# Kernel tuning notes

Hardware: AMD Instinct MI355X
Metric: run time of the kernel (lower is better)

## Reference

```python
import jax, jax.numpy as jnp
import numpy as np
from jax.scipy.linalg import solve_triangular

B = 131072; OBS = 128; AD = 8; H = 64; FH = 32; NL = 4
D1 = AD // 2; D2 = AD - D1; TRIL = AD * (AD + 1) // 2
_rows, _cols = np.tril_indices(AD)          # same row-major order as torch.tril_indices
_diag = (_rows == _cols)                    # bool mask over TRIL entries
_diag_pos = np.where(_diag)[0]
LOG2PI = float(np.log(2.0 * np.pi))
EPS = float(np.finfo(np.float32).eps)       # torch RMSNorm default eps = finfo.eps


def _rms(x, w):
    return x * jax.lax.rsqrt(jnp.mean(x * x, axis=-1, keepdims=True) + EPS) * w


def setup_inputs() -> dict:
    ks = iter(jax.random.split(jax.random.key(0), 32))
    def w(shape, scale):
        return jax.random.normal(next(ks), shape, jnp.float32) * scale
    z = lambda *s: jnp.zeros(s, jnp.float32)
    return dict(
        x=jax.random.normal(next(ks), (B, OBS), jnp.float32),
        action=jax.random.normal(next(ks), (B, AD), jnp.float32),
        z_rpo=jax.random.uniform(next(ks), (B, AD), jnp.float32, -0.1, 0.1),
        cW1=w((OBS, H), OBS ** -0.5), cb1=z(H), c_rms=jnp.ones(H, jnp.float32),
        cW2=w((H, H), H ** -0.5), cb2=z(H), cW3=w((H, 1), H ** -0.5), cb3=z(1),
        aW1=w((OBS, H), OBS ** -0.5), ab1=z(H), aW2=w((H, H), H ** -0.5), ab2=z(H),
        mW=w((H, AD), 0.01), mb=z(AD),
        tW1=w((OBS, H), OBS ** -0.5), tb1=z(H), t_rms1=jnp.ones(H, jnp.float32),
        tW2=w((H, H), H ** -0.5), tb2=z(H), t_rms2=jnp.ones(H, jnp.float32),
        hW=w((H, TRIL), 0.01), hb=z(TRIL),
        fW1=w((NL, D1 + OBS, FH), (D1 + OBS) ** -0.5), fb1=z(NL, FH),
        fW2=w((NL, FH, 2 * D2), 0.01), fb2=z(NL, 2 * D2),
    )


def reference(x, action, z_rpo, cW1, cb1, c_rms, cW2, cb2, cW3, cb3,
              aW1, ab1, aW2, ab2, mW, mb,
              tW1, tb1, t_rms1, tW2, tb2, t_rms2, hW, hb,
              fW1, fb1, fW2, fb2):
    silu = jax.nn.silu
    Bn = x.shape[0]
    # actor mean trunk + head, with RPO uniform perturbation (action is given)
    h = silu(silu(x @ aW1 + ab1) @ aW2 + ab2)
    action_mean = h @ mW + mb + z_rpo
    # state-dependent lower-triangular covariance factor
    tl = _rms(silu(x @ tW1 + tb1), t_rms1)
    tl = _rms(silu(tl @ tW2 + tb2), t_rms2)
    raw = tl @ hW + hb                                   # [B, TRIL]
    proc = jnp.where(_diag, jax.nn.softplus(raw), raw)
    L = jnp.zeros((Bn, AD, AD), raw.dtype).at[:, _rows, _cols].set(proc)
    log_det_L = jnp.log(proc[:, _diag_pos]).sum(-1)      # [B]
    # coupling flow inverse: noise -> correlated
    noise = action - action_mean
    x1, x2 = noise[:, :D1], noise[:, D1:]
    fld = jnp.zeros((Bn,), raw.dtype)
    for i in reversed(range(NL)):
        cond, y = (x1, x2) if i % 2 == 0 else (x2, x1)
        st = silu(jnp.concatenate([cond, x], -1) @ fW1[i] + fb1[i]) @ fW2[i] + fb2[i]
        s_raw, tshift = jnp.split(st, 2, -1)
        s = jnp.tanh(s_raw) * 2.0
        xt = (y - tshift) * jnp.exp(-s)
        if i % 2 == 0:
            x2 = xt
        else:
            x1 = xt
        fld = fld + s.sum(-1)
    correlated = jnp.concatenate([x1, x2], -1)           # [B, AD]
    zc = solve_triangular(L, correlated[..., None], lower=True)[..., 0]
    mahal = (zc * zc).sum(-1)
    log_prob = -0.5 * (AD * LOG2PI + mahal) - log_det_L - fld
    entropy = 0.5 * (AD * (1.0 + LOG2PI)) + log_det_L + fld
    # critic
    v = _rms(silu(x @ cW1 + cb1), c_rms)
    v = silu(v @ cW2 + cb2) @ cW3 + cb3                  # [B, 1]
    return (action, log_prob, entropy, v)
```

## Files before the change

kernel.cpp:

```cpp
#include <hip/hip_runtime.h>

typedef __attribute__((ext_vector_type(8))) short    v8s;
typedef __attribute__((ext_vector_type(4))) float    f4;
typedef __attribute__((ext_vector_type(2))) float    f2;
typedef __attribute__((ext_vector_type(2))) unsigned u32x2;

#define MFMA16 __builtin_amdgcn_mfma_f32_16x16x32_bf16

#define AW1T 0
#define TW1T 8192
#define CW1T 16384
#define AW2T 24576
#define TW2T 28672
#define CW2T 32768
#define MWT  36864
#define HWT  37888
#define FW1XT 40960
#define FW2T  57344
#define WS_BF16_TOTAL 59392
#define W1CTO 0
#define HBPO  512

#define LOG2PI 1.83787706640934548356f
#define EPSF   1.1920928955078125e-07f

__device__ __constant__ int PERM[36] = {0,2,5,9,14,20,27,35,
  1,3,4,6,7,8,10,11,12,13,15,16,17,18,19,21,22,23,24,25,26,28,29,30,31,32,33,34};

__device__ __forceinline__ float ubits(unsigned u){union{unsigned u;float f;}c;c.u=u;return c.f;}
__device__ __forceinline__ unsigned fbits(float f){union{float f;unsigned u;}c;c.f=f;return c.u;}
__device__ __forceinline__ float rcpf(float x){ return __builtin_amdgcn_rcpf(x); }
__device__ __forceinline__ float siluf(float v){ return v * rcpf(1.f + __expf(-v)); }
__device__ __forceinline__ unsigned pk2(float a,float b){
  unsigned ua=fbits(a); ua+=0x7fffu+((ua>>16)&1u);
  unsigned ub=fbits(b); ub+=0x7fffu+((ub>>16)&1u);
  return (ua>>16)|(ub&0xffff0000u);
}
__device__ __forceinline__ unsigned short f2bu(float a){
  unsigned ua=fbits(a); ua+=0x7fffu+((ua>>16)&1u);
  return (unsigned short)(ua>>16);
}
__device__ __forceinline__ float b2f16(unsigned short h){ return ubits(((unsigned)h)<<16); }
__device__ __forceinline__ float qsum(float v){
  v += __shfl_xor(v,16,64); v += __shfl_xor(v,32,64); return v;
}
__device__ __forceinline__ int swz(int row, int blk){ return row*64 + ((blk ^ (row&7))*8); }
__device__ __forceinline__ int swzx(int row, int blk){ return row*128 + ((blk ^ (row&7))*8); }

__global__ __launch_bounds__(256)
void prep_kernel(const float* __restrict__ aW1, const float* __restrict__ aW2,
                 const float* __restrict__ mW,  const float* __restrict__ tW1,
                 const float* __restrict__ tW2, const float* __restrict__ hW,
                 const float* __restrict__ hb,  const float* __restrict__ cW1,
                 const float* __restrict__ cW2, const float* __restrict__ fW1,
                 const float* __restrict__ fW2,
                 unsigned short* __restrict__ ws16, float* __restrict__ wsf)
{
  const int tid = blockIdx.x*256 + threadIdx.x;
  const int stride = gridDim.x*256;
  for (int idx=tid; idx<64*128; idx+=stride){
    int f=idx>>9, r=idx&511, lane=r>>3, j=idx&7;
    int wt=f>>2, kt=f&3, c=lane&15, q=lane>>4;
    int n=wt*16+c, k=kt*32+q*8+j;
    ws16[AW1T+idx]=f2bu(aW1[k*64+n]);
    ws16[TW1T+idx]=f2bu(tW1[k*64+n]);
    ws16[CW1T+idx]=f2bu(cW1[k*64+n]);
  }
  for (int idx=tid; idx<64*64; idx+=stride){
    int f=idx>>9, r=idx&511, lane=r>>3, j=idx&7;
    int wt=f>>1, kt=f&1, c=lane&15, q=lane>>4;
    int n=wt*16+c, k=kt*32+q*8+j;
    ws16[AW2T+idx]=f2bu(aW2[k*64+n]);
    ws16[TW2T+idx]=f2bu(tW2[k*64+n]);
    ws16[CW2T+idx]=f2bu(cW2[k*64+n]);
  }
  for (int idx=tid; idx<16*64; idx+=stride){
    int f=idx>>9, r=idx&511, lane=r>>3, j=idx&7;
    int kt=f, c=lane&15, q=lane>>4;
    int n=c, k=kt*32+q*8+j;
    ws16[MWT+idx]=f2bu(n<8 ? mW[k*8+n] : 0.f);
  }
  for (int idx=tid; idx<48*64; idx+=stride){
    int f=idx>>9, r=idx&511, lane=r>>3, j=idx&7;
    int wt=f>>1, kt=f&1, c=lane&15, q=lane>>4;
    int n=wt*16+c, k=kt*32+q*8+j;
    ws16[HWT+idx]=f2bu(n<36 ? hW[k*36+PERM[n]] : 0.f);
  }
  for (int idx=tid; idx<4*32*128; idx+=stride){
    int i=idx>>12, rem=idx&4095;
    int f=rem>>9, r=rem&511, lane=r>>3, j=idx&7;
    int wt=f>>2, kt=f&3, c=lane&15, q=lane>>4;
    int n=wt*16+c, k=kt*32+q*8+j;
    ws16[FW1XT+idx]=f2bu(fW1[i*4224 + (4+k)*32 + n]);
  }
  for (int idx=tid; idx<4*16*32; idx+=stride){
    int i=idx>>9, r=idx&511, lane=r>>3, j=idx&7;
    int c=lane&15, q=lane>>4;
    int k=q*8+j;
    ws16[FW2T+idx]=f2bu(c<8 ? fW2[i*256 + k*8 + c] : 0.f);
  }
  for (int idx=tid; idx<4*32*4; idx+=stride){
    int i=idx>>7, rem=idx&127, n=rem>>2, k=rem&3;
    wsf[W1CTO+idx]=fW1[i*4224 + k*32 + n];
  }
  for (int idx=tid; idx<48; idx+=stride)
    wsf[HBPO+idx] = idx<36 ? hb[PERM[idx]] : 0.f;
}

template<int NWT>
__device__ __forceinline__ void gemmX(const unsigned short* __restrict__ Wt,
                                      const v8s* __restrict__ xf,
                                      f4 (*acc)[2], int lane)
{
#pragma unroll
  for (int kt=0; kt<4; ++kt){
    v8s wf[NWT];
#pragma unroll
    for (int wt=0; wt<NWT; ++wt)
      wf[wt] = *(const v8s*)(Wt + ((wt*4 + kt)*64 + lane)*8);
#pragma unroll
    for (int wt=0; wt<NWT; ++wt)
#pragma unroll
      for (int et=0; et<2; ++et)
        acc[wt][et] = MFMA16(wf[wt], xf[et*4+kt], acc[wt][et], 0,0,0);
  }
}

template<int NWT>
__device__ __forceinline__ void gemmH(const unsigned short* __restrict__ Wt,
                                      const unsigned short* __restrict__ actL,
                                      f4 (*acc)[2], int lane, int c, int q)
{
#pragma unroll
  for (int kt=0; kt<2; ++kt){
    v8s wf[NWT];
#pragma unroll
    for (int wt=0; wt<NWT; ++wt)
      wf[wt] = *(const v8s*)(Wt + ((wt*2 + kt)*64 + lane)*8);
    v8s af[2];
#pragma unroll
    for (int et=0; et<2; ++et)
      af[et] = *(const v8s*)(actL + swz(et*16+c, kt*4+q));
#pragma unroll
    for (int wt=0; wt<NWT; ++wt)
#pragma unroll
      for (int et=0; et<2; ++et)
        acc[wt][et] = MFMA16(wf[wt], af[et], acc[wt][et], 0,0,0);
  }
}

__global__ __launch_bounds__(64) __attribute__((amdgpu_waves_per_eu(3, 4)))
void policy_kernel(
    const float* __restrict__ x,    const float* __restrict__ action, const float* __restrict__ z_rpo,
    const float* __restrict__ cb1,  const float* __restrict__ c_rms,  const float* __restrict__ cb2,
    const float* __restrict__ cW3,  const float* __restrict__ cb3,
    const float* __restrict__ ab1,  const float* __restrict__ ab2,    const float* __restrict__ mb,
    const float* __restrict__ tb1,  const float* __restrict__ t_rms1, const float* __restrict__ tb2,
    const float* __restrict__ t_rms2,
    const float* __restrict__ fb1,  const float* __restrict__ fb2,
    const unsigned short* __restrict__ ws16, const float* __restrict__ wsf,
    float* __restrict__ out, const int Btot)
{
  const int lane = threadIdx.x;
  const int q = lane >> 4, c = lane & 15;
  const int b0 = blockIdx.x << 5;

  __shared__ alignas(16) unsigned char smem[8192];
  unsigned short* actL = (unsigned short*)smem;
  unsigned short* hidL = (unsigned short*)smem;
  unsigned short* triL = (unsigned short*)(smem + 4096);
  float*          nstL = (float*)(smem + 6400);
  unsigned short* amL  = (unsigned short*)(smem + 7424);
  unsigned short* xL   = (unsigned short*)smem;

  v8s xf[8];
  {
    const float* xb = x + (size_t)b0*128;
    const int rr = lane>>3, bb = (lane&7)*2;
#pragma unroll
    for (int rg=0; rg<4; ++rg){
      const int row = rg*8 + rr;
      const float* p = xb + row*128 + (lane&7)*16;
      f4 u0=*(const f4*)p, u1=*(const f4*)(p+4), u2=*(const f4*)(p+8), u3=*(const f4*)(p+12);
      union { unsigned u[4]; v8s v; } r0, r1;
      r0.u[0]=pk2(u0[0],u0[1]); r0.u[1]=pk2(u0[2],u0[3]);
      r0.u[2]=pk2(u1[0],u1[1]); r0.u[3]=pk2(u1[2],u1[3]);
      r1.u[0]=pk2(u2[0],u2[1]); r1.u[1]=pk2(u2[2],u2[3]);
      r1.u[2]=pk2(u3[0],u3[1]); r1.u[3]=pk2(u3[2],u3[3]);
      *(v8s*)(xL + swzx(row, bb  )) = r0.v;
      *(v8s*)(xL + swzx(row, bb+1)) = r1.v;
    }
    __syncthreads();
#pragma unroll
    for (int et=0; et<2; ++et)
#pragma unroll
      for (int kt=0; kt<4; ++kt)
        xf[et*4+kt] = *(const v8s*)(xL + swzx(et*16+c, kt*4+q));
  }

  f4 acc[4][2];
  const f4 z4 = {0.f,0.f,0.f,0.f};

#pragma unroll
  for (int wt=0; wt<4; ++wt) for (int et=0; et<2; ++et) acc[wt][et]=z4;
  gemmX<4>(ws16+AW1T, xf, acc, lane);
#pragma unroll
  for (int wt=0; wt<4; ++wt){
    const f4 bv = *(const f4*)(ab1 + wt*16 + q*4);
#pragma unroll
    for (int et=0; et<2; ++et){
      float s0=siluf(acc[wt][et][0]+bv[0]), s1=siluf(acc[wt][et][1]+bv[1]);
      float s2=siluf(acc[wt][et][2]+bv[2]), s3=siluf(acc[wt][et][3]+bv[3]);
      u32x2 u = {pk2(s0,s1), pk2(s2,s3)};
      *(u32x2*)(actL + swz(et*16+c, wt*2+(q>>1)) + (q&1)*4) = u;
    }
  }
#pragma unroll
  for (int wt=0; wt<4; ++wt) for (int et=0; et<2; ++et) acc[wt][et]=z4;
  gemmH<4>(ws16+AW2T, actL, acc, lane, c, q);
#pragma unroll
  for (int wt=0; wt<4; ++wt){
    const f4 bv = *(const f4*)(ab2 + wt*16 + q*4);
#pragma unroll
    for (int et=0; et<2; ++et){
      float s0=siluf(acc[wt][et][0]+bv[0]), s1=siluf(acc[wt][et][1]+bv[1]);
      float s2=siluf(acc[wt][et][2]+bv[2]), s3=siluf(acc[wt][et][3]+bv[3]);
      u32x2 u = {pk2(s0,s1), pk2(s2,s3)};
      *(u32x2*)(actL + swz(et*16+c, wt*2+(q>>1)) + (q&1)*4) = u;
    }
  }
  {
    f4 am1[1][2]; am1[0][0]=z4; am1[0][1]=z4;
    gemmH<1>(ws16+MWT, actL, am1, lane, c, q);
    if (q<2){
      const f4 mbv = *(const f4*)(mb + q*4);
#pragma unroll
      for (int et=0; et<2; ++et){
        u32x2 u = {pk2(am1[0][et][0]+mbv[0], am1[0][et][1]+mbv[1]),
                   pk2(am1[0][et][2]+mbv[2], am1[0][et][3]+mbv[3])};
        *(u32x2*)(amL + (et*16+c)*8 + q*4) = u;
      }
    }
  }

#pragma unroll
  for (int wt=0; wt<4; ++wt) for (int et=0; et<2; ++et) acc[wt][et]=z4;
  gemmX<4>(ws16+TW1T, xf, acc, lane);
  float r1[2];
  {
    float ss[2]={0.f,0.f};
#pragma unroll
    for (int wt=0; wt<4; ++wt){
      const f4 bv = *(const f4*)(tb1 + wt*16 + q*4);
      const f4 rw = *(const f4*)(t_rms1 + wt*16 + q*4);
#pragma unroll
      for (int et=0; et<2; ++et){
        float s0=siluf(acc[wt][et][0]+bv[0]), s1=siluf(acc[wt][et][1]+bv[1]);
        float s2=siluf(acc[wt][et][2]+bv[2]), s3=siluf(acc[wt][et][3]+bv[3]);
        ss[et] += s0*s0+s1*s1+s2*s2+s3*s3;
        u32x2 u = {pk2(s0*rw[0],s1*rw[1]), pk2(s2*rw[2],s3*rw[3])};
        *(u32x2*)(actL + swz(et*16+c, wt*2+(q>>1)) + (q&1)*4) = u;
      }
    }
#pragma unroll
    for (int et=0; et<2; ++et) r1[et]=rsqrtf(qsum(ss[et])*(1.f/64.f)+EPSF);
  }
#pragma unroll
  for (int wt=0; wt<4; ++wt) for (int et=0; et<2; ++et) acc[wt][et]=z4;
  gemmH<4>(ws16+TW2T, actL, acc, lane, c, q);
  float r2[2];
  {
    float ss[2]={0.f,0.f};
#pragma unroll
    for (int wt=0; wt<4; ++wt){
      const f4 bv = *(const f4*)(tb2 + wt*16 + q*4);
      const f4 rw = *(const f4*)(t_rms2 + wt*16 + q*4);
#pragma unroll
      for (int et=0; et<2; ++et){
        float s0=siluf(r1[et]*acc[wt][et][0]+bv[0]), s1=siluf(r1[et]*acc[wt][et][1]+bv[1]);
        float s2=siluf(r1[et]*acc[wt][et][2]+bv[2]), s3=siluf(r1[et]*acc[wt][et][3]+bv[3]);
        ss[et] += s0*s0+s1*s1+s2*s2+s3*s3;
        u32x2 u = {pk2(s0*rw[0],s1*rw[1]), pk2(s2*rw[2],s3*rw[3])};
        *(u32x2*)(actL + swz(et*16+c, wt*2+(q>>1)) + (q&1)*4) = u;
      }
    }
#pragma unroll
    for (int et=0; et<2; ++et) r2[et]=rsqrtf(qsum(ss[et])*(1.f/64.f)+EPSF);
  }
  float ldet[2];
  {
    f4 a3[3][2];
#pragma unroll
    for (int wt=0; wt<3; ++wt) for (int et=0; et<2; ++et) a3[wt][et]=z4;
    gemmH<3>(ws16+HWT, actL, a3, lane, c, q);
    float ldp[2]={0.f,0.f};
#pragma unroll
    for (int wt=0; wt<3; ++wt){
      const f4 hbv = *(const f4*)(wsf + HBPO + wt*16 + q*4);
#pragma unroll
      for (int et=0; et<2; ++et){
        float t0=r2[et]*a3[wt][et][0]+hbv[0], t1=r2[et]*a3[wt][et][1]+hbv[1];
        float t2=r2[et]*a3[wt][et][2]+hbv[2], t3=r2[et]*a3[wt][et][3]+hbv[3];
        if (wt==0 && q<2){
          t0=fmaxf(t0,0.f)+__logf(1.f+__expf(-fabsf(t0)));
          t1=fmaxf(t1,0.f)+__logf(1.f+__expf(-fabsf(t1)));
          t2=fmaxf(t2,0.f)+__logf(1.f+__expf(-fabsf(t2)));
          t3=fmaxf(t3,0.f)+__logf(1.f+__expf(-fabsf(t3)));
          ldp[et] += __logf(t0)+__logf(t1)+__logf(t2)+__logf(t3);
        }
        if (wt<2 || q==0){
          u32x2 u = {pk2(t0,t1), pk2(t2,t3)};
          *(u32x2*)(triL + (et*16+c)*36 + wt*16 + q*4) = u;
        }
      }
    }
#pragma unroll
    for (int et=0; et<2; ++et) ldet[et]=qsum(ldp[et]);
  }

#pragma unroll
  for (int wt=0; wt<4; ++wt) for (int et=0; et<2; ++et) acc[wt][et]=z4;
  gemmX<4>(ws16+CW1T, xf, acc, lane);
  float rc[2];
  {
    float ss[2]={0.f,0.f};
#pragma unroll
    for (int wt=0; wt<4; ++wt){
      const f4 bv = *(const f4*)(cb1 + wt*16 + q*4);
      const f4 rw = *(const f4*)(c_rms + wt*16 + q*4);
#pragma unroll
      for (int et=0; et<2; ++et){
        float s0=siluf(acc[wt][et][0]+bv[0]), s1=siluf(acc[wt][et][1]+bv[1]);
        float s2=siluf(acc[wt][et][2]+bv[2]), s3=siluf(acc[wt][et][3]+bv[3]);
        ss[et] += s0*s0+s1*s1+s2*s2+s3*s3;
        u32x2 u = {pk2(s0*rw[0],s1*rw[1]), pk2(s2*rw[2],s3*rw[3])};
        *(u32x2*)(actL + swz(et*16+c, wt*2+(q>>1)) + (q&1)*4) = u;
      }
    }
#pragma unroll
    for (int et=0; et<2; ++et) rc[et]=rsqrtf(qsum(ss[et])*(1.f/64.f)+EPSF);
  }
  float vv[2];
  {
#pragma unroll
    for (int wt=0; wt<4; ++wt) for (int et=0; et<2; ++et) acc[wt][et]=z4;
    gemmH<4>(ws16+CW2T, actL, acc, lane, c, q);
    float vp[2]={0.f,0.f};
#pragma unroll
    for (int wt=0; wt<4; ++wt){
      const f4 bv = *(const f4*)(cb2 + wt*16 + q*4);
      const f4 wv = *(const f4*)(cW3 + wt*16 + q*4);
#pragma unroll
      for (int et=0; et<2; ++et){
        vp[et] = fmaf(siluf(rc[et]*acc[wt][et][0]+bv[0]), wv[0], vp[et]);
        vp[et] = fmaf(siluf(rc[et]*acc[wt][et][1]+bv[1]), wv[1], vp[et]);
        vp[et] = fmaf(siluf(rc[et]*acc[wt][et][2]+bv[2]), wv[2], vp[et]);
        vp[et] = fmaf(siluf(rc[et]*acc[wt][et][3]+bv[3]), wv[3], vp[et]);
      }
    }
    const float cb3v = cb3[0];
#pragma unroll
    for (int et=0; et<2; ++et) vv[et]=qsum(vp[et])+cb3v;
  }

  const int l = lane;
  float nst[8], fld=0.f;
  if (l < 32){
    const size_t bb = (size_t)(b0+l)*8;
    f4 a0=*(const f4*)(action+bb), a1=*(const f4*)(action+bb+4);
    f4 zr0=*(const f4*)(z_rpo+bb), zr1=*(const f4*)(z_rpo+bb+4);
    *(f4*)(out+bb)=a0; *(f4*)(out+bb+4)=a1;
#pragma unroll
    for (int j=0;j<4;++j){
      nst[j]   = a0[j]-b2f16(amL[l*8+j])  -zr0[j];
      nst[4+j] = a1[j]-b2f16(amL[l*8+4+j])-zr1[j];
    }
    *(f4*)(nstL + l*8)     = (f4){nst[0],nst[1],nst[2],nst[3]};
    *(f4*)(nstL + l*8 + 4) = (f4){nst[4],nst[5],nst[6],nst[7]};
  }

#pragma unroll
  for (int ii=0; ii<4; ++ii){
    const int i = 3-ii;
    const int cb = (i&1)?4:0, yb = (i&1)?0:4;
    f4 a2[2][2];
#pragma unroll
    for (int wt=0; wt<2; ++wt) for (int et=0; et<2; ++et) a2[wt][et]=z4;
    gemmX<2>(ws16+FW1XT+i*4096, xf, a2, lane);
    float nv[2][4];
#pragma unroll
    for (int et=0; et<2; ++et){
      const float* np = nstL + (et*16+c)*8 + cb;
      f2 t0=*(const f2*)np, t1=*(const f2*)(np+2);
      nv[et][0]=t0[0]; nv[et][1]=t0[1]; nv[et][2]=t1[0]; nv[et][3]=t1[1];
    }
#pragma unroll
    for (int wt=0; wt<2; ++wt){
      const f4 bv = *(const f4*)(fb1 + i*32 + wt*16 + q*4);
      float sh[2][4];
#pragma unroll
      for (int r=0; r<4; ++r){
        const f4 wc = *(const f4*)(wsf + W1CTO + i*128 + (wt*16+q*4+r)*4);
#pragma unroll
        for (int et=0; et<2; ++et){
          float hv = a2[wt][et][r] + bv[r]
                   + wc[0]*nv[et][0] + wc[1]*nv[et][1]
                   + wc[2]*nv[et][2] + wc[3]*nv[et][3];
          sh[et][r] = siluf(hv);
        }
      }
#pragma unroll
      for (int et=0; et<2; ++et){
        u32x2 u = {pk2(sh[et][0],sh[et][1]), pk2(sh[et][2],sh[et][3])};
        *(u32x2*)(hidL + swz(et*16+c, wt*2+(q>>1)) + (q&1)*4) = u;
      }
    }
    {
      const v8s wf3 = *(const v8s*)(ws16 + FW2T + i*512 + lane*8);
      f4 as[2];
#pragma unroll
      for (int et=0; et<2; ++et){
        const v8s hf = *(const v8s*)(hidL + swz(et*16+c, q));
        f4 a1s = z4;
        a1s = MFMA16(wf3, hf, a1s, 0,0,0);
        as[et]=a1s;
      }
      if (q<2){
        const f4 fbv = *(const f4*)(fb2 + i*8 + q*4);
#pragma unroll
        for (int et=0; et<2; ++et){
          u32x2 u = {pk2(as[et][0]+fbv[0], as[et][1]+fbv[1]),
                     pk2(as[et][2]+fbv[2], as[et][3]+fbv[3])};
          *(u32x2*)(amL + (et*16+c)*8 + q*4) = u;
        }
      }
    }
    if (l < 32){
      float sr0=b2f16(amL[l*8+0]), sr1=b2f16(amL[l*8+1]);
      float sr2=b2f16(amL[l*8+2]), sr3=b2f16(amL[l*8+3]);
      float th0=b2f16(amL[l*8+4]), th1=b2f16(amL[l*8+5]);
      float th2=b2f16(amL[l*8+6]), th3=b2f16(amL[l*8+7]);
      float s0=2.f-4.f*rcpf(__expf(2.f*sr0)+1.f);
      float s1=2.f-4.f*rcpf(__expf(2.f*sr1)+1.f);
      float s2=2.f-4.f*rcpf(__expf(2.f*sr2)+1.f);
      float s3=2.f-4.f*rcpf(__expf(2.f*sr3)+1.f);
      nst[yb+0]=(nst[yb+0]-th0)*__expf(-s0);
      nst[yb+1]=(nst[yb+1]-th1)*__expf(-s1);
      nst[yb+2]=(nst[yb+2]-th2)*__expf(-s2);
      nst[yb+3]=(nst[yb+3]-th3)*__expf(-s3);
      *(f4*)(nstL + l*8 + yb) = (f4){nst[yb+0],nst[yb+1],nst[yb+2],nst[yb+3]};
      fld += s0+s1+s2+s3;
    }
  }

  if (l < 32){
    constexpr int INVPERM[36] = {0,8,1,9,10,2,11,12,13,3,14,15,16,17,4,18,19,20,
                                 21,22,5,23,24,25,26,27,28,6,29,30,31,32,33,34,35,7};
    float tri[36];
#pragma unroll
    for (int j=0;j<36;++j) tri[j] = b2f16(triL[l*36 + INVPERM[j]]);
    float zv[8], mahal=0.f;
#pragma unroll
    for (int r=0;r<8;++r){
      float s=nst[r];
      const int base=(r*(r+1))>>1;
#pragma unroll
      for (int cc=0;cc<r;++cc) s -= tri[base+cc]*zv[cc];
      const float z = s*rcpf(tri[base+r]);
      zv[r]=z; mahal+=z*z;
    }
    const float ldet_s = (l<16)?ldet[0]:ldet[1];
    const float v_s    = (l<16)?vv[0]:vv[1];
    const float lp = -0.5f*(8.f*LOG2PI+mahal) - ldet_s - fld;
    const float en =  0.5f*(8.f*(1.f+LOG2PI)) + ldet_s + fld;
    out[(size_t)Btot*8  + b0 + l] = lp;
    out[(size_t)Btot*9  + b0 + l] = en;
    out[(size_t)Btot*10 + b0 + l] = v_s;
  }
}

extern "C" void kernel_launch(void* const* d_in, const int* in_sizes, int n_in,
                              void* d_out, int out_size, void* d_ws, size_t ws_size,
                              hipStream_t stream) {
  const float* x      = (const float*)d_in[0];
  const float* action = (const float*)d_in[1];
  const float* z_rpo  = (const float*)d_in[2];
  const float* cW1    = (const float*)d_in[3];
  const float* cb1    = (const float*)d_in[4];
  const float* c_rms  = (const float*)d_in[5];
  const float* cW2    = (const float*)d_in[6];
  const float* cb2    = (const float*)d_in[7];
  const float* cW3    = (const float*)d_in[8];
  const float* cb3    = (const float*)d_in[9];
  const float* aW1    = (const float*)d_in[10];
  const float* ab1    = (const float*)d_in[11];
  const float* aW2    = (const float*)d_in[12];
  const float* ab2    = (const float*)d_in[13];
  const float* mW     = (const float*)d_in[14];
  const float* mb     = (const float*)d_in[15];
  const float* tW1    = (const float*)d_in[16];
  const float* tb1    = (const float*)d_in[17];
  const float* t_rms1 = (const float*)d_in[18];
  const float* tW2    = (const float*)d_in[19];
  const float* tb2    = (const float*)d_in[20];
  const float* t_rms2 = (const float*)d_in[21];
  const float* hW     = (const float*)d_in[22];
  const float* hb     = (const float*)d_in[23];
  const float* fW1    = (const float*)d_in[24];
  const float* fb1    = (const float*)d_in[25];
  const float* fW2    = (const float*)d_in[26];
  const float* fb2    = (const float*)d_in[27];
  float* out = (float*)d_out;

  unsigned short* ws16 = (unsigned short*)d_ws;
  float* wsf = (float*)((char*)d_ws + WS_BF16_TOTAL*2);

  const int Btot = in_sizes[0] / 128;

  hipLaunchKernelGGL(prep_kernel, dim3(128), dim3(256), 0, stream,
                     aW1, aW2, mW, tW1, tW2, hW, hb, cW1, cW2, fW1, fW2, ws16, wsf);
  hipLaunchKernelGGL(policy_kernel, dim3(Btot/32), dim3(64), 0, stream,
                     x, action, z_rpo, cb1, c_rms, cb2, cW3, cb3,
                     ab1, ab2, mb, tb1, t_rms1, tb2, t_rms2, fb1, fb2,
                     ws16, wsf, out, Btot);
}
```

Before: 191.0 us.

## Split policy kernel into two specialized waves per block

Each block now has two waves instead of one. Wave 0 runs the actor trunk and the serial coupling-flow chain. Wave 1 precomputes the x-dependent flow first-layer products into LDS, then runs the tril head and the critic, and finally does the triangular solve and writes the outputs. The aim is to shorten the per-block serial dependency chain by overlapping independent MLP branches. In exchange, LDS grows from 8 KB to about 29 KB per block and extra barriers are added, which can lower occupancy and leave one wave idle if the two halves are unbalanced.

```diff
diff --git a/kernel.cpp b/kernel.cpp
--- a/kernel.cpp
+++ b/kernel.cpp
@@ -149,7 +149,7 @@
   }
 }
 
-__global__ __launch_bounds__(64) __attribute__((amdgpu_waves_per_eu(3, 4)))
+__global__ __launch_bounds__(128) __attribute__((amdgpu_waves_per_eu(3, 4)))
 void policy_kernel(
     const float* __restrict__ x,    const float* __restrict__ action, const float* __restrict__ z_rpo,
     const float* __restrict__ cb1,  const float* __restrict__ c_rms,  const float* __restrict__ cb2,
@@ -161,25 +161,28 @@
     const unsigned short* __restrict__ ws16, const float* __restrict__ wsf,
     float* __restrict__ out, const int Btot)
 {
-  const int lane = threadIdx.x;
+  const int tid  = threadIdx.x;
+  const int wv   = tid >> 6;
+  const int lane = tid & 63;
   const int q = lane >> 4, c = lane & 15;
   const int b0 = blockIdx.x << 5;
 
-  __shared__ alignas(16) unsigned char smem[8192];
-  unsigned short* actL = (unsigned short*)smem;
-  unsigned short* hidL = (unsigned short*)smem;
-  unsigned short* triL = (unsigned short*)(smem + 4096);
-  float*          nstL = (float*)(smem + 6400);
-  unsigned short* amL  = (unsigned short*)(smem + 7424);
+  __shared__ alignas(16) unsigned char smem[29056];
+  float*          a2L  = (float*)smem;
   unsigned short* xL   = (unsigned short*)smem;
-
-  v8s xf[8];
+  unsigned short* act0 = (unsigned short*)(smem + 16896);
+  unsigned short* act1 = (unsigned short*)(smem + 20992);
+  unsigned short* triL = (unsigned short*)(smem + 25088);
+  float*          nstL = (float*)(smem + 27392);
+  unsigned short* amL  = (unsigned short*)(smem + 28416);
+  float*          fldL = (float*)(smem + 28928);
+
   {
     const float* xb = x + (size_t)b0*128;
     const int rr = lane>>3, bb = (lane&7)*2;
 #pragma unroll
-    for (int rg=0; rg<4; ++rg){
-      const int row = rg*8 + rr;
+    for (int rg=0; rg<2; ++rg){
+      const int row = wv*16 + rg*8 + rr;
       const float* p = xb + row*128 + (lane&7)*16;
       f4 u0=*(const f4*)p, u1=*(const f4*)(p+4), u2=*(const f4*)(p+8), u3=*(const f4*)(p+12);
       union { unsigned u[4]; v8s v; } r0, r1;
@@ -190,182 +193,84 @@
       *(v8s*)(xL + swzx(row, bb  )) = r0.v;
       *(v8s*)(xL + swzx(row, bb+1)) = r1.v;
     }
-    __syncthreads();
-#pragma unroll
-    for (int et=0; et<2; ++et)
-#pragma unroll
-      for (int kt=0; kt<4; ++kt)
-        xf[et*4+kt] = *(const v8s*)(xL + swzx(et*16+c, kt*4+q));
-  }
+  }
+  __syncthreads();
+  v8s xf[8];
+#pragma unroll
+  for (int et=0; et<2; ++et)
+#pragma unroll
+    for (int kt=0; kt<4; ++kt)
+      xf[et*4+kt] = *(const v8s*)(xL + swzx(et*16+c, kt*4+q));
+  __syncthreads();
 
   f4 acc[4][2];
   const f4 z4 = {0.f,0.f,0.f,0.f};
-
-#pragma unroll
-  for (int wt=0; wt<4; ++wt) for (int et=0; et<2; ++et) acc[wt][et]=z4;
-  gemmX<4>(ws16+AW1T, xf, acc, lane);
-#pragma unroll
-  for (int wt=0; wt<4; ++wt){
-    const f4 bv = *(const f4*)(ab1 + wt*16 + q*4);
-#pragma unroll
-    for (int et=0; et<2; ++et){
-      float s0=siluf(acc[wt][et][0]+bv[0]), s1=siluf(acc[wt][et][1]+bv[1]);
-      float s2=siluf(acc[wt][et][2]+bv[2]), s3=siluf(acc[wt][et][3]+bv[3]);
-      u32x2 u = {pk2(s0,s1), pk2(s2,s3)};
-      *(u32x2*)(actL + swz(et*16+c, wt*2+(q>>1)) + (q&1)*4) = u;
-    }
-  }
-#pragma unroll
-  for (int wt=0; wt<4; ++wt) for (int et=0; et<2; ++et) acc[wt][et]=z4;
-  gemmH<4>(ws16+AW2T, actL, acc, lane, c, q);
-#pragma unroll
-  for (int wt=0; wt<4; ++wt){
-    const f4 bv = *(const f4*)(ab2 + wt*16 + q*4);
-#pragma unroll
-    for (int et=0; et<2; ++et){
-      float s0=siluf(acc[wt][et][0]+bv[0]), s1=siluf(acc[wt][et][1]+bv[1]);
-      float s2=siluf(acc[wt][et][2]+bv[2]), s3=siluf(acc[wt][et][3]+bv[3]);
-      u32x2 u = {pk2(s0,s1), pk2(s2,s3)};
-      *(u32x2*)(actL + swz(et*16+c, wt*2+(q>>1)) + (q&1)*4) = u;
-    }
-  }
-  {
-    f4 am1[1][2]; am1[0][0]=z4; am1[0][1]=z4;
-    gemmH<1>(ws16+MWT, actL, am1, lane, c, q);
-    if (q<2){
-      const f4 mbv = *(const f4*)(mb + q*4);
-#pragma unroll
-      for (int et=0; et<2; ++et){
-        u32x2 u = {pk2(am1[0][et][0]+mbv[0], am1[0][et][1]+mbv[1]),
-                   pk2(am1[0][et][2]+mbv[2], am1[0][et][3]+mbv[3])};
-        *(u32x2*)(amL + (et*16+c)*8 + q*4) = u;
-      }
-    }
-  }
-
-#pragma unroll
-  for (int wt=0; wt<4; ++wt) for (int et=0; et<2; ++et) acc[wt][et]=z4;
-  gemmX<4>(ws16+TW1T, xf, acc, lane);
-  float r1[2];
-  {
-    float ss[2]={0.f,0.f};
+  const int l = lane;
+  float ldet[2], vv[2];
+
+  if (wv == 0){
+#pragma unroll
+    for (int wt=0; wt<4; ++wt) for (int et=0; et<2; ++et) acc[wt][et]=z4;
+    gemmX<4>(ws16+AW1T, xf, acc, lane);
 #pragma unroll
     for (int wt=0; wt<4; ++wt){
-      const f4 bv = *(const f4*)(tb1 + wt*16 + q*4);
-      const f4 rw = *(const f4*)(t_rms1 + wt*16 + q*4);
+      const f4 bv = *(const f4*)(ab1 + wt*16 + q*4);
 #pragma unroll
       for (int et=0; et<2; ++et){
         float s0=siluf(acc[wt][et][0]+bv[0]), s1=siluf(acc[wt][et][1]+bv[1]);
         float s2=siluf(acc[wt][et][2]+bv[2]), s3=siluf(acc[wt][et][3]+bv[3]);
-        ss[et] += s0*s0+s1*s1+s2*s2+s3*s3;
-        u32x2 u = {pk2(s0*rw[0],s1*rw[1]), pk2(s2*rw[2],s3*rw[3])};
-        *(u32x2*)(actL + swz(et*16+c, wt*2+(q>>1)) + (q&1)*4) = u;
-      }
-    }
-#pragma unroll
-    for (int et=0; et<2; ++et) r1[et]=rsqrtf(qsum(ss[et])*(1.f/64.f)+EPSF);
-  }
-#pragma unroll
-  for (int wt=0; wt<4; ++wt) for (int et=0; et<2; ++et) acc[wt][et]=z4;
-  gemmH<4>(ws16+TW2T, actL, acc, lane, c, q);
-  float r2[2];
-  {
-    float ss[2]={0.f,0.f};
+        u32x2 u = {pk2(s0,s1), pk2(s2,s3)};
+        *(u32x2*)(act0 + swz(et*16+c, wt*2+(q>>1)) + (q&1)*4) = u;
+      }
+    }
+#pragma unroll
+    for (int wt=0; wt<4; ++wt) for (int et=0; et<2; ++et) acc[wt][et]=z4;
+    gemmH<4>(ws16+AW2T, act0, acc, lane, c, q);
 #pragma unroll
     for (int wt=0; wt<4; ++wt){
-      const f4 bv = *(const f4*)(tb2 + wt*16 + q*4);
-      const f4 rw = *(const f4*)(t_rms2 + wt*16 + q*4);
-#pragma unroll
-      for (int et=0; et<2; ++et){
-        float s0=siluf(r1[et]*acc[wt][et][0]+bv[0]), s1=siluf(r1[et]*acc[wt][et][1]+bv[1]);
-        float s2=siluf(r1[et]*acc[wt][et][2]+bv[2]), s3=siluf(r1[et]*acc[wt][et][3]+bv[3]);
-        ss[et] += s0*s0+s1*s1+s2*s2+s3*s3;
-        u32x2 u = {pk2(s0*rw[0],s1*rw[1]), pk2(s2*rw[2],s3*rw[3])};
-        *(u32x2*)(actL + swz(et*16+c, wt*2+(q>>1)) + (q&1)*4) = u;
-      }
-    }
-#pragma unroll
-    for (int et=0; et<2; ++et) r2[et]=rsqrtf(qsum(ss[et])*(1.f/64.f)+EPSF);
-  }
-  float ldet[2];
-  {
-    f4 a3[3][2];
-#pragma unroll
-    for (int wt=0; wt<3; ++wt) for (int et=0; et<2; ++et) a3[wt][et]=z4;
-    gemmH<3>(ws16+HWT, actL, a3, lane, c, q);
-    float ldp[2]={0.f,0.f};
-#pragma unroll
-    for (int wt=0; wt<3; ++wt){
-      const f4 hbv = *(const f4*)(wsf + HBPO + wt*16 + q*4);
-#pragma unroll
-      for (int et=0; et<2; ++et){
-        float t0=r2[et]*a3[wt][et][0]+hbv[0], t1=r2[et]*a3[wt][et][1]+hbv[1];
-        float t2=r2[et]*a3[wt][et][2]+hbv[2], t3=r2[et]*a3[wt][et][3]+hbv[3];
-        if (wt==0 && q<2){
-          t0=fmaxf(t0,0.f)+__logf(1.f+__expf(-fabsf(t0)));
-          t1=fmaxf(t1,0.f)+__logf(1.f+__expf(-fabsf(t1)));
-          t2=fmaxf(t2,0.f)+__logf(1.f+__expf(-fabsf(t2)));
-          t3=fmaxf(t3,0.f)+__logf(1.f+__expf(-fabsf(t3)));
-          ldp[et] += __logf(t0)+__logf(t1)+__logf(t2)+__logf(t3);
-        }
-        if (wt<2 || q==0){
-          u32x2 u = {pk2(t0,t1), pk2(t2,t3)};
-          *(u32x2*)(triL + (et*16+c)*36 + wt*16 + q*4) = u;
-        }
-      }
-    }
-#pragma unroll
-    for (int et=0; et<2; ++et) ldet[et]=qsum(ldp[et]);
-  }
-
-#pragma unroll
-  for (int wt=0; wt<4; ++wt) for (int et=0; et<2; ++et) acc[wt][et]=z4;
-  gemmX<4>(ws16+CW1T, xf, acc, lane);
-  float rc[2];
-  {
-    float ss[2]={0.f,0.f};
-#pragma unroll
-    for (int wt=0; wt<4; ++wt){
-      const f4 bv = *(const f4*)(cb1 + wt*16 + q*4);
-      const f4 rw = *(const f4*)(c_rms + wt*16 + q*4);
+      const f4 bv = *(const f4*)(ab2 + wt*16 + q*4);
 #pragma unroll
       for (int et=0; et<2; ++et){
         float s0=siluf(acc[wt][et][0]+bv[0]), s1=siluf(acc[wt][et][1]+bv[1]);
         float s2=siluf(acc[wt][et][2]+bv[2]), s3=siluf(acc[wt][et][3]+bv[3]);
-        ss[et] += s0*s0+s1*s1+s2*s2+s3*s3;
-        u32x2 u = {pk2(s0*rw[0],s1*rw[1]), pk2(s2*rw[2],s3*rw[3])};
-        *(u32x2*)(actL + swz(et*16+c, wt*2+(q>>1)) + (q&1)*4) = u;
-      }
-    }
-#pragma unroll
-    for (int et=0; et<2; ++et) rc[et]=rsqrtf(qsum(ss[et])*(1.f/64.f)+EPSF);
-  }
-  float vv[2];
-  {
-#pragma unroll
-    for (int wt=0; wt<4; ++wt) for (int et=0; et<2; ++et) acc[wt][et]=z4;
-    gemmH<4>(ws16+CW2T, actL, acc, lane, c, q);
-    float vp[2]={0.f,0.f};
-#pragma unroll
-    for (int wt=0; wt<4; ++wt){
-      const f4 bv = *(const f4*)(cb2 + wt*16 + q*4);
-      const f4 wv = *(const f4*)(cW3 + wt*16 + q*4);
-#pragma unroll
-      for (int et=0; et<2; ++et){
-        vp[et] = fmaf(siluf(rc[et]*acc[wt][et][0]+bv[0]), wv[0], vp[et]);
-        vp[et] = fmaf(siluf(rc[et]*acc[wt][et][1]+bv[1]), wv[1], vp[et]);
-        vp[et] = fmaf(siluf(rc[et]*acc[wt][et][2]+bv[2]), wv[2], vp[et]);
-        vp[et] = fmaf(siluf(rc[et]*acc[wt][et][3]+bv[3]), wv[3], vp[et]);
-      }
-    }
-    const float cb3v = cb3[0];
-#pragma unroll
-    for (int et=0; et<2; ++et) vv[et]=qsum(vp[et])+cb3v;
-  }
-
-  const int l = lane;
+        u32x2 u = {pk2(s0,s1), pk2(s2,s3)};
+        *(u32x2*)(act0 + swz(et*16+c, wt*2+(q>>1)) + (q&1)*4) = u;
+      }
+    }
+    {
+      f4 am1[1][2]; am1[0][0]=z4; am1[0][1]=z4;
+      gemmH<1>(ws16+MWT, act0, am1, lane, c, q);
+      if (q<2){
+        const f4 mbv = *(const f4*)(mb + q*4);
+#pragma unroll
+        for (int et=0; et<2; ++et){
+          u32x2 u = {pk2(am1[0][et][0]+mbv[0], am1[0][et][1]+mbv[1]),
+                     pk2(am1[0][et][2]+mbv[2], am1[0][et][3]+mbv[3])};
+          *(u32x2*)(amL + (et*16+c)*8 + q*4) = u;
+        }
+      }
+    }
+  } else {
+#pragma unroll
+    for (int i=0; i<4; ++i){
+      f4 a2[2][2];
+#pragma unroll
+      for (int wt=0; wt<2; ++wt) for (int et=0; et<2; ++et) a2[wt][et]=z4;
+      gemmX<2>(ws16+FW1XT+i*4096, xf, a2, lane);
+#pragma unroll
+      for (int wt=0; wt<2; ++wt)
+#pragma unroll
+        for (int r=0; r<4; ++r){
+          const int n = wt*16 + q*4 + r;
+#pragma unroll
+          for (int et=0; et<2; ++et)
+            a2L[(i*32 + n)*33 + et*16 + c] = a2[wt][et][r];
+        }
+    }
+  }
+
   float nst[8], fld=0.f;
-  if (l < 32){
+  if (wv==0 && l<32){
     const size_t bb = (size_t)(b0+l)*8;
     f4 a0=*(const f4*)(action+bb), a1=*(const f4*)(action+bb+4);
     f4 zr0=*(const f4*)(z_rpo+bb), zr1=*(const f4*)(z_rpo+bb+4);
@@ -379,90 +284,215 @@
     *(f4*)(nstL + l*8 + 4) = (f4){nst[4],nst[5],nst[6],nst[7]};
   }
 
-#pragma unroll
-  for (int ii=0; ii<4; ++ii){
-    const int i = 3-ii;
-    const int cb = (i&1)?4:0, yb = (i&1)?0:4;
-    f4 a2[2][2];
-#pragma unroll
-    for (int wt=0; wt<2; ++wt) for (int et=0; et<2; ++et) a2[wt][et]=z4;
-    gemmX<2>(ws16+FW1XT+i*4096, xf, a2, lane);
-    float nv[2][4];
-#pragma unroll
-    for (int et=0; et<2; ++et){
-      const float* np = nstL + (et*16+c)*8 + cb;
-      f2 t0=*(const f2*)np, t1=*(const f2*)(np+2);
-      nv[et][0]=t0[0]; nv[et][1]=t0[1]; nv[et][2]=t1[0]; nv[et][3]=t1[1];
-    }
-#pragma unroll
-    for (int wt=0; wt<2; ++wt){
-      const f4 bv = *(const f4*)(fb1 + i*32 + wt*16 + q*4);
-      float sh[2][4];
-#pragma unroll
-      for (int r=0; r<4; ++r){
-        const f4 wc = *(const f4*)(wsf + W1CTO + i*128 + (wt*16+q*4+r)*4);
-#pragma unroll
-        for (int et=0; et<2; ++et){
-          float hv = a2[wt][et][r] + bv[r]
-                   + wc[0]*nv[et][0] + wc[1]*nv[et][1]
-                   + wc[2]*nv[et][2] + wc[3]*nv[et][3];
-          sh[et][r] = siluf(hv);
-        }
-      }
+  __syncthreads();
+
+  if (wv == 0){
+#pragma unroll
+    for (int ii=0; ii<4; ++ii){
+      const int i = 3-ii;
+      const int cb = (i&1)?4:0, yb = (i&1)?0:4;
+      float nv[2][4];
 #pragma unroll
       for (int et=0; et<2; ++et){
-        u32x2 u = {pk2(sh[et][0],sh[et][1]), pk2(sh[et][2],sh[et][3])};
-        *(u32x2*)(hidL + swz(et*16+c, wt*2+(q>>1)) + (q&1)*4) = u;
-      }
-    }
+        const float* np = nstL + (et*16+c)*8 + cb;
+        f2 t0=*(const f2*)np, t1=*(const f2*)(np+2);
+        nv[et][0]=t0[0]; nv[et][1]=t0[1]; nv[et][2]=t1[0]; nv[et][3]=t1[1];
+      }
+#pragma unroll
+      for (int wt=0; wt<2; ++wt){
+        const f4 bv = *(const f4*)(fb1 + i*32 + wt*16 + q*4);
+        float sh[2][4];
+#pragma unroll
+        for (int r=0; r<4; ++r){
+          const int n = wt*16 + q*4 + r;
+          const f4 wc = *(const f4*)(wsf + W1CTO + i*128 + n*4);
+#pragma unroll
+          for (int et=0; et<2; ++et){
+            float hv = a2L[(i*32 + n)*33 + et*16 + c] + bv[r]
+                     + wc[0]*nv[et][0] + wc[1]*nv[et][1]
+                     + wc[2]*nv[et][2] + wc[3]*nv[et][3];
+            sh[et][r] = siluf(hv);
+          }
+        }
+#pragma unroll
+        for (int et=0; et<2; ++et){
+          u32x2 u = {pk2(sh[et][0],sh[et][1]), pk2(sh[et][2],sh[et][3])};
+          *(u32x2*)(act0 + swz(et*16+c, wt*2+(q>>1)) + (q&1)*4) = u;
+        }
+      }
+      {
+        const v8s wf3 = *(const v8s*)(ws16 + FW2T + i*512 + lane*8);
+        f4 as[2];
+#pragma unroll
+        for (int et=0; et<2; ++et){
+          const v8s hf = *(const v8s*)(act0 + swz(et*16+c, q));
+          f4 a1s = z4;
+          a1s = MFMA16(wf3, hf, a1s, 0,0,0);
+          as[et]=a1s;
+        }
+        if (q<2){
+          const f4 fbv = *(const f4*)(fb2 + i*8 + q*4);
+#pragma unroll
+          for (int et=0; et<2; ++et){
+            u32x2 u = {pk2(as[et][0]+fbv[0], as[et][1]+fbv[1]),
+                       pk2(as[et][2]+fbv[2], as[et][3]+fbv[3])};
+            *(u32x2*)(amL + (et*16+c)*8 + q*4) = u;
+          }
+        }
+      }
+      if (l < 32){
+        float sr0=b2f16(amL[l*8+0]), sr1=b2f16(amL[l*8+1]);
+        float sr2=b2f16(amL[l*8+2]), sr3=b2f16(amL[l*8+3]);
+        float th0=b2f16(amL[l*8+4]), th1=b2f16(amL[l*8+5]);
+        float th2=b2f16(amL[l*8+6]), th3=b2f16(amL[l*8+7]);
+        float s0=2.f-4.f*rcpf(__expf(2.f*sr0)+1.f);
+        float s1=2.f-4.f*rcpf(__expf(2.f*sr1)+1.f);
+        float s2=2.f-4.f*rcpf(__expf(2.f*sr2)+1.f);
+        float s3=2.f-4.f*rcpf(__expf(2.f*sr3)+1.f);
+        nst[yb+0]=(nst[yb+0]-th0)*__expf(-s0);
+        nst[yb+1]=(nst[yb+1]-th1)*__expf(-s1);
+        nst[yb+2]=(nst[yb+2]-th2)*__expf(-s2);
+        nst[yb+3]=(nst[yb+3]-th3)*__expf(-s3);
+        *(f4*)(nstL + l*8 + yb) = (f4){nst[yb+0],nst[yb+1],nst[yb+2],nst[yb+3]};
+        fld += s0+s1+s2+s3;
+      }
+    }
+    if (l < 32) fldL[l] = fld;
+  } else {
+#pragma unroll
+    for (int wt=0; wt<4; ++wt) for (int et=0; et<2; ++et) acc[wt][et]=z4;
+    gemmX<4>(ws16+TW1T, xf, acc, lane);
+    float r1[2];
     {
-      const v8s wf3 = *(const v8s*)(ws16 + FW2T + i*512 + lane*8);
-      f4 as[2];
-#pragma unroll
-      for (int et=0; et<2; ++et){
-        const v8s hf = *(const v8s*)(hidL + swz(et*16+c, q));
-        f4 a1s = z4;
-        a1s = MFMA16(wf3, hf, a1s, 0,0,0);
-        as[et]=a1s;
-      }
-      if (q<2){
-        const f4 fbv = *(const f4*)(fb2 + i*8 + q*4);
-#pragma unroll
-        for (int et=0; et<2; ++et){
-          u32x2 u = {pk2(as[et][0]+fbv[0], as[et][1]+fbv[1]),
-                     pk2(as[et][2]+fbv[2], as[et][3]+fbv[3])};
-          *(u32x2*)(amL + (et*16+c)*8 + q*4) = u;
-        }
-      }
-    }
-    if (l < 32){
-      float sr0=b2f16(amL[l*8+0]), sr1=b2f16(amL[l*8+1]);
-      float sr2=b2f16(amL[l*8+2]), sr3=b2f16(amL[l*8+3]);
-      float th0=b2f16(amL[l*8+4]), th1=b2f16(amL[l*8+5]);
-      float th2=b2f16(amL[l*8+6]), th3=b2f16(amL[l*8+7]);
-      float s0=2.f-4.f*rcpf(__expf(2.f*sr0)+1.f);
-      float s1=2.f-4.f*rcpf(__expf(2.f*sr1)+1.f);
-      float s2=2.f-4.f*rcpf(__expf(2.f*sr2)+1.f);
-      float s3=2.f-4.f*rcpf(__expf(2.f*sr3)+1.f);
-      nst[yb+0]=(nst[yb+0]-th0)*__expf(-s0);
-      nst[yb+1]=(nst[yb+1]-th1)*__expf(-s1);
-      nst[yb+2]=(nst[yb+2]-th2)*__expf(-s2);
-      nst[yb+3]=(nst[yb+3]-th3)*__expf(-s3);
-      *(f4*)(nstL + l*8 + yb) = (f4){nst[yb+0],nst[yb+1],nst[yb+2],nst[yb+3]};
-      fld += s0+s1+s2+s3;
-    }
-  }
-
-  if (l < 32){
+      float ss[2]={0.f,0.f};
+#pragma unroll
+      for (int wt=0; wt<4; ++wt){
+        const f4 bv = *(const f4*)(tb1 + wt*16 + q*4);
+        const f4 rw = *(const f4*)(t_rms1 + wt*16 + q*4);
+#pragma unroll
+        for (int et=0; et<2; ++et){
+          float s0=siluf(acc[wt][et][0]+bv[0]), s1=siluf(acc[wt][et][1]+bv[1]);
+          float s2=siluf(acc[wt][et][2]+bv[2]), s3=siluf(acc[wt][et][3]+bv[3]);
+          ss[et] += s0*s0+s1*s1+s2*s2+s3*s3;
+          u32x2 u = {pk2(s0*rw[0],s1*rw[1]), pk2(s2*rw[2],s3*rw[3])};
+          *(u32x2*)(act1 + swz(et*16+c, wt*2+(q>>1)) + (q&1)*4) = u;
+        }
+      }
+#pragma unroll
+      for (int et=0; et<2; ++et) r1[et]=rsqrtf(qsum(ss[et])*(1.f/64.f)+EPSF);
+    }
+#pragma unroll
+    for (int wt=0; wt<4; ++wt) for (int et=0; et<2; ++et) acc[wt][et]=z4;
+    gemmH<4>(ws16+TW2T, act1, acc, lane, c, q);
+    float r2[2];
+    {
+      float ss[2]={0.f,0.f};
+#pragma unroll
+      for (int wt=0; wt<4; ++wt){
+        const f4 bv = *(const f4*)(tb2 + wt*16 + q*4);
+        const f4 rw = *(const f4*)(t_rms2 + wt*16 + q*4);
+#pragma unroll
+        for (int et=0; et<2; ++et){
+          float s0=siluf(r1[et]*acc[wt][et][0]+bv[0]), s1=siluf(r1[et]*acc[wt][et][1]+bv[1]);
+          float s2=siluf(r1[et]*acc[wt][et][2]+bv[2]), s3=siluf(r1[et]*acc[wt][et][3]+bv[3]);
+          ss[et] += s0*s0+s1*s1+s2*s2+s3*s3;
+          u32x2 u = {pk2(s0*rw[0],s1*rw[1]), pk2(s2*rw[2],s3*rw[3])};
+          *(u32x2*)(act1 + swz(et*16+c, wt*2+(q>>1)) + (q&1)*4) = u;
+        }
+      }
+#pragma unroll
+      for (int et=0; et<2; ++et) r2[et]=rsqrtf(qsum(ss[et])*(1.f/64.f)+EPSF);
+    }
+    {
+      f4 a3[3][2];
+#pragma unroll
+      for (int wt=0; wt<3; ++wt) for (int et=0; et<2; ++et) a3[wt][et]=z4;
+      gemmH<3>(ws16+HWT, act1, a3, lane, c, q);
+      float ldp[2]={0.f,0.f};
+#pragma unroll
+      for (int wt=0; wt<3; ++wt){
+        const f4 hbv = *(const f4*)(wsf + HBPO + wt*16 + q*4);
+#pragma unroll
+        for (int et=0; et<2; ++et){
+          float t0=r2[et]*a3[wt][et][0]+hbv[0], t1=r2[et]*a3[wt][et][1]+hbv[1];
+          float t2=r2[et]*a3[wt][et][2]+hbv[2], t3=r2[et]*a3[wt][et][3]+hbv[3];
+          if (wt==0 && q<2){
+            t0=fmaxf(t0,0.f)+__logf(1.f+__expf(-fabsf(t0)));
+            t1=fmaxf(t1,0.f)+__logf(1.f+__expf(-fabsf(t1)));
+            t2=fmaxf(t2,0.f)+__logf(1.f+__expf(-fabsf(t2)));
+            t3=fmaxf(t3,0.f)+__logf(1.f+__expf(-fabsf(t3)));
+            ldp[et] += __logf(t0)+__logf(t1)+__logf(t2)+__logf(t3);
+          }
+          if (wt<2 || q==0){
+            u32x2 u = {pk2(t0,t1), pk2(t2,t3)};
+            *(u32x2*)(triL + (et*16+c)*36 + wt*16 + q*4) = u;
+          }
+        }
+      }
+#pragma unroll
+      for (int et=0; et<2; ++et) ldet[et]=qsum(ldp[et]);
+    }
+#pragma unroll
+    for (int wt=0; wt<4; ++wt) for (int et=0; et<2; ++et) acc[wt][et]=z4;
+    gemmX<4>(ws16+CW1T, xf, acc, lane);
+    float rc[2];
+    {
+      float ss[2]={0.f,0.f};
+#pragma unroll
+      for (int wt=0; wt<4; ++wt){
+        const f4 bv = *(const f4*)(cb1 + wt*16 + q*4);
+        const f4 rw = *(const f4*)(c_rms + wt*16 + q*4);
+#pragma unroll
+        for (int et=0; et<2; ++et){
+          float s0=siluf(acc[wt][et][0]+bv[0]), s1=siluf(acc[wt][et][1]+bv[1]);
+          float s2=siluf(acc[wt][et][2]+bv[2]), s3=siluf(acc[wt][et][3]+bv[3]);
+          ss[et] += s0*s0+s1*s1+s2*s2+s3*s3;
+          u32x2 u = {pk2(s0*rw[0],s1*rw[1]), pk2(s2*rw[2],s3*rw[3])};
+          *(u32x2*)(act1 + swz(et*16+c, wt*2+(q>>1)) + (q&1)*4) = u;
+        }
+      }
+#pragma unroll
+      for (int et=0; et<2; ++et) rc[et]=rsqrtf(qsum(ss[et])*(1.f/64.f)+EPSF);
+    }
+    {
+#pragma unroll
+      for (int wt=0; wt<4; ++wt) for (int et=0; et<2; ++et) acc[wt][et]=z4;
+      gemmH<4>(ws16+CW2T, act1, acc, lane, c, q);
+      float vp[2]={0.f,0.f};
+#pragma unroll
+      for (int wt=0; wt<4; ++wt){
+        const f4 bv = *(const f4*)(cb2 + wt*16 + q*4);
+        const f4 wvv = *(const f4*)(cW3 + wt*16 + q*4);
+#pragma unroll
+        for (int et=0; et<2; ++et){
+          vp[et] = fmaf(siluf(rc[et]*acc[wt][et][0]+bv[0]), wvv[0], vp[et]);
+          vp[et] = fmaf(siluf(rc[et]*acc[wt][et][1]+bv[1]), wvv[1], vp[et]);
+          vp[et] = fmaf(siluf(rc[et]*acc[wt][et][2]+bv[2]), wvv[2], vp[et]);
+          vp[et] = fmaf(siluf(rc[et]*acc[wt][et][3]+bv[3]), wvv[3], vp[et]);
+        }
+      }
+      const float cb3v = cb3[0];
+#pragma unroll
+      for (int et=0; et<2; ++et) vv[et]=qsum(vp[et])+cb3v;
+    }
+  }
+
+  __syncthreads();
+
+  if (wv==1 && l<32){
     constexpr int INVPERM[36] = {0,8,1,9,10,2,11,12,13,3,14,15,16,17,4,18,19,20,
                                  21,22,5,23,24,25,26,27,28,6,29,30,31,32,33,34,35,7};
     float tri[36];
 #pragma unroll
     for (int j=0;j<36;++j) tri[j] = b2f16(triL[l*36 + INVPERM[j]]);
+    float nf[8];
+#pragma unroll
+    for (int j=0;j<8;++j) nf[j] = nstL[l*8+j];
+    const float fldv = fldL[l];
     float zv[8], mahal=0.f;
 #pragma unroll
     for (int r=0;r<8;++r){
-      float s=nst[r];
+      float s=nf[r];
       const int base=(r*(r+1))>>1;
 #pragma unroll
       for (int cc=0;cc<r;++cc) s -= tri[base+cc]*zv[cc];
@@ -471,8 +501,8 @@
     }
     const float ldet_s = (l<16)?ldet[0]:ldet[1];
     const float v_s    = (l<16)?vv[0]:vv[1];
-    const float lp = -0.5f*(8.f*LOG2PI+mahal) - ldet_s - fld;
-    const float en =  0.5f*(8.f*(1.f+LOG2PI)) + ldet_s + fld;
+    const float lp = -0.5f*(8.f*LOG2PI+mahal) - ldet_s - fldv;
+    const float en =  0.5f*(8.f*(1.f+LOG2PI)) + ldet_s + fldv;
     out[(size_t)Btot*8  + b0 + l] = lp;
     out[(size_t)Btot*9  + b0 + l] = en;
     out[(size_t)Btot*10 + b0 + l] = v_s;
@@ -519,7 +549,7 @@
 
   hipLaunchKernelGGL(prep_kernel, dim3(128), dim3(256), 0, stream,
                      aW1, aW2, mW, tW1, tW2, hW, hb, cW1, cW2, fW1, fW2, ws16, wsf);
-  hipLaunchKernelGGL(policy_kernel, dim3(Btot/32), dim3(64), 0, stream,
+  hipLaunchKernelGGL(policy_kernel, dim3(Btot/32), dim3(128), 0, stream,
                      x, action, z_rpo, cb1, c_rms, cb2, cW3, cb3,
                      ab1, ab2, mb, tb1, t_rms1, tb2, t_rms2, fb1, fb2,
                      ws16, wsf, out, Btot);
```

Measured after the change: 200.7 us. 5.1% more time.
